# Performance work log

Hardware: AMD Instinct MI355X
Metric: run time of the kernel (lower is better)

## Reference

```python
import jax, jax.numpy as jnp
import numpy as np
from jax import lax

ALPHA_LO = float(np.exp(-1.0 / 5.0))
ALPHA_HI = float(np.exp(-1.0 / 25.0))
THRESHOLD = 1.0


def setup_inputs() -> dict:
    key = jax.random.key(0)
    k1, k2, k3, k4, k5 = jax.random.split(key, 5)
    B, T, I, H = 64, 1024, 512, 512
    x = jax.random.normal(k1, (B, T, I), dtype=jnp.float32)
    # kaiming-uniform-like small init for Linear weight
    bound = 1.0 / np.sqrt(I)
    W = jax.random.uniform(k2, (H, I), minval=-bound, maxval=bound, dtype=jnp.float32)
    alpha = ALPHA_LO + jax.random.uniform(k3, (H,), dtype=jnp.float32) * (ALPHA_HI - ALPHA_LO)
    u0 = jax.random.uniform(k4, (B, H), dtype=jnp.float32)
    s0 = jax.random.uniform(k5, (B, H), dtype=jnp.float32)
    return {"x": x, "W": W, "alpha": alpha, "u0": u0, "s0": s0}


def reference(x, W, alpha, u0, s0):
    # x: [B, T, I], W: [H, I] (torch Linear layout), alpha/u0/s0 over H
    al = jnp.clip(alpha, ALPHA_LO, ALPHA_HI)  # [H]
    Wx = jnp.einsum('bti,hi->bth', x, W)      # [B, T, H]

    def step(carry, wx_t):
        u, s = carry
        u = al * (u - s) + (1.0 - al) * wx_t
        s = (u - THRESHOLD > 0).astype(wx_t.dtype)
        return (u, s), s

    _, spikes = lax.scan(step, (u0, s0), jnp.swapaxes(Wx, 0, 1))  # [T, B, H]
    return jnp.swapaxes(spikes, 0, 1)  # [B, T, H]
```

## Files before the change

### kernel.cpp

```cpp
#include <hip/hip_runtime.h>
#include <hip/hip_bf16.h>


#define ALPHA_LO_F 0.8187307530779818f
#define ALPHA_HI_F 0.9607894391523232f

typedef float v2f __attribute__((ext_vector_type(2)));

#define T_DIM 1024
#define K_DIM 512
#define H_DIM 512
#define CT    256
#define CH    128
#define NCHK  (T_DIM / CT)
#define BK    16
#define APAD  260
#define BPAD  132

__global__ __launch_bounds__(512, 1) void lif_fused(
    const float* __restrict__ x,
    const float* __restrict__ W,
    const float* __restrict__ alpha,
    const float* __restrict__ u0,
    const float* __restrict__ s0,
    float* __restrict__ out)
{
    __shared__ float As[BK][APAD];
    __shared__ float Bs[BK][BPAD];
    __shared__ float u_s[CH], s_s[CH], al_s[CH];

    const int tid = threadIdx.x;
    const int b   = blockIdx.x & 63;
    const int hc  = blockIdx.x >> 6;
    const int h0  = hc * CH;

    if (tid < CH) {
        const int h = h0 + tid;
        float a = alpha[h];
        al_s[tid] = fminf(fmaxf(a, ALPHA_LO_F), ALPHA_HI_F);
        u_s[tid] = u0[(size_t)b * H_DIM + h];
        s_s[tid] = s0[(size_t)b * H_DIM + h];
    }

    const int tm = tid >> 4;
    const int tn = tid & 15;

    const float* xb = x + (size_t)b * T_DIM * K_DIM;
    const float* Wc = W + (size_t)h0 * K_DIM;

    __syncthreads();

    for (int c = 0; c < NCHK; ++c) {
        const int t0 = c * CT;

        v2f acc[8][4] = {};

        for (int k0 = 0; k0 < K_DIM; k0 += BK) {
            #pragma unroll
            for (int r = 0; r < 3; ++r) {
                const int fid = tid + r * 512;
                if (fid < 1024) {
                    const int row = fid >> 2;
                    const int kq  = (fid & 3) * 4;
                    float4 v = *(const float4*)(xb + (size_t)(t0 + row) * K_DIM + k0 + kq);
                    As[kq + 0][row] = v.x;  As[kq + 1][row] = v.y;
                    As[kq + 2][row] = v.z;  As[kq + 3][row] = v.w;
                } else {
                    const int g   = fid - 1024;
                    const int row = g >> 2;
                    const int kq  = (g & 3) * 4;
                    float4 v = *(const float4*)(Wc + (size_t)row * K_DIM + k0 + kq);
                    Bs[kq + 0][row] = v.x;  Bs[kq + 1][row] = v.y;
                    Bs[kq + 2][row] = v.z;  Bs[kq + 3][row] = v.w;
                }
            }
            __syncthreads();

            #pragma unroll
            for (int k = 0; k < BK; ++k) {
                const float* Ak = &As[k][tm * 8];
                const float* Bk = &Bs[k][tn * 8];
                float4 a0 = *(const float4*)(Ak);
                float4 a1 = *(const float4*)(Ak + 4);
                float4 b0 = *(const float4*)(Bk);
                float4 b1 = *(const float4*)(Bk + 4);
                v2f bb[4];
                bb[0] = (v2f){b0.x, b0.y};  bb[1] = (v2f){b0.z, b0.w};
                bb[2] = (v2f){b1.x, b1.y};  bb[3] = (v2f){b1.z, b1.w};
                float a[8] = {a0.x, a0.y, a0.z, a0.w, a1.x, a1.y, a1.z, a1.w};
                #pragma unroll
                for (int i = 0; i < 8; ++i) {
                    v2f ai = (v2f){a[i], a[i]};
                    #pragma unroll
                    for (int jv = 0; jv < 4; ++jv)
                        acc[i][jv] = __builtin_elementwise_fma(ai, bb[jv], acc[i][jv]);
                }
            }
            __syncthreads();
        }

        for (int stage = 0; stage < 32; ++stage) {
            if (tm == stage) {
                const int hb = tn * 8;
                float u[8], s[8], av[8], om[8];
                #pragma unroll
                for (int j = 0; j < 8; ++j) {
                    u[j]  = u_s[hb + j];
                    s[j]  = s_s[hb + j];
                    av[j] = al_s[hb + j];
                    om[j] = 1.0f - av[j];
                }
                #pragma unroll
                for (int i = 0; i < 8; ++i) {
                    float wx[8] = {acc[i][0].x, acc[i][0].y, acc[i][1].x, acc[i][1].y,
                                   acc[i][2].x, acc[i][2].y, acc[i][3].x, acc[i][3].y};
                    #pragma unroll
                    for (int j = 0; j < 8; ++j) {
                        u[j] = av[j] * (u[j] - s[j]) + om[j] * wx[j];
                        s[j] = (u[j] - 1.0f > 0.0f) ? 1.0f : 0.0f;
                    }
                    const int t = t0 + stage * 8 + i;
                    float* orow = out + ((size_t)b * T_DIM + t) * H_DIM + h0 + hb;
                    *(float4*)(orow)     = make_float4(s[0], s[1], s[2], s[3]);
                    *(float4*)(orow + 4) = make_float4(s[4], s[5], s[6], s[7]);
                }
                #pragma unroll
                for (int j = 0; j < 8; ++j) {
                    u_s[hb + j] = u[j];
                    s_s[hb + j] = s[j];
                }
            }
            __syncthreads();
        }
    }
}

extern "C" void kernel_launch(void* const* d_in, const int* in_sizes, int n_in,
                              void* d_out, int out_size, void* d_ws, size_t ws_size,
                              hipStream_t stream) {
    const float* x     = (const float*)d_in[0];
    const float* W     = (const float*)d_in[1];
    const float* alpha = (const float*)d_in[2];
    const float* u0    = (const float*)d_in[3];
    const float* s0    = (const float*)d_in[4];
    float* out = (float*)d_out;

    const int H = in_sizes[2];
    const int B = in_sizes[3] / H;
    const int grid = (H_DIM / CH) * B;

    lif_fused<<<grid, 512, 0, stream>>>(x, W, alpha, u0, s0, out);
}
```

Measured before the change: 726.0 us.

## Double-buffer LDS tiles with register prefetch and halve H chunk per block

Adds register prefetch of the next K tile (and of the next time chunk's first tile) together with double-buffered shared-memory tiles, so global loads overlap the FMA loop and one barrier per K step is dropped. The block is shrunk to 256 threads covering 64 H columns, which doubles the grid and lets two blocks share a CU. In exchange, each x tile is now loaded by twice as many blocks, and the serial recurrence stage still runs one thread row at a time.

```diff
diff --git a/kernel.cpp b/kernel.cpp
--- a/kernel.cpp
+++ b/kernel.cpp
@@ -11,13 +11,13 @@
 #define K_DIM 512
 #define H_DIM 512
 #define CT    256
-#define CH    128
+#define CH    64
 #define NCHK  (T_DIM / CT)
 #define BK    16
 #define APAD  260
-#define BPAD  132
+#define BPAD  68
 
-__global__ __launch_bounds__(512, 1) void lif_fused(
+__global__ __launch_bounds__(256, 2) void lif_fused(
     const float* __restrict__ x,
     const float* __restrict__ W,
     const float* __restrict__ alpha,
@@ -25,8 +25,8 @@
     const float* __restrict__ s0,
     float* __restrict__ out)
 {
-    __shared__ float As[BK][APAD];
-    __shared__ float Bs[BK][BPAD];
+    __shared__ float As[2][BK][APAD];
+    __shared__ float Bs[2][BK][BPAD];
     __shared__ float u_s[CH], s_s[CH], al_s[CH];
 
     const int tid = threadIdx.x;
@@ -42,44 +42,64 @@
         s_s[tid] = s0[(size_t)b * H_DIM + h];
     }
 
-    const int tm = tid >> 4;
-    const int tn = tid & 15;
+    const int tm = tid >> 3;
+    const int tn = tid & 7;
+
+    const int arow = tid >> 2;
+    const int akq  = (tid & 3) * 4;
+    const int brow = tid >> 2;
+    const int bkq  = (tid & 3) * 4;
 
     const float* xb = x + (size_t)b * T_DIM * K_DIM;
     const float* Wc = W + (size_t)h0 * K_DIM;
+
+    float4 aR[4]; float4 bR;
+
+    {
+        #pragma unroll
+        for (int r = 0; r < 4; ++r)
+            aR[r] = *(const float4*)(xb + (size_t)(arow + r * 64) * K_DIM + akq);
+        bR = *(const float4*)(Wc + (size_t)brow * K_DIM + bkq);
+    }
 
     __syncthreads();
 
     for (int c = 0; c < NCHK; ++c) {
         const int t0 = c * CT;
 
+        #pragma unroll
+        for (int r = 0; r < 4; ++r) {
+            const int row = arow + r * 64;
+            As[0][akq + 0][row] = aR[r].x;  As[0][akq + 1][row] = aR[r].y;
+            As[0][akq + 2][row] = aR[r].z;  As[0][akq + 3][row] = aR[r].w;
+        }
+        Bs[0][bkq + 0][brow] = bR.x;  Bs[0][bkq + 1][brow] = bR.y;
+        Bs[0][bkq + 2][brow] = bR.z;  Bs[0][bkq + 3][brow] = bR.w;
+        __syncthreads();
+
         v2f acc[8][4] = {};
 
-        for (int k0 = 0; k0 < K_DIM; k0 += BK) {
-            #pragma unroll
-            for (int r = 0; r < 3; ++r) {
-                const int fid = tid + r * 512;
-                if (fid < 1024) {
-                    const int row = fid >> 2;
-                    const int kq  = (fid & 3) * 4;
-                    float4 v = *(const float4*)(xb + (size_t)(t0 + row) * K_DIM + k0 + kq);
-                    As[kq + 0][row] = v.x;  As[kq + 1][row] = v.y;
-                    As[kq + 2][row] = v.z;  As[kq + 3][row] = v.w;
-                } else {
-                    const int g   = fid - 1024;
-                    const int row = g >> 2;
-                    const int kq  = (g & 3) * 4;
-                    float4 v = *(const float4*)(Wc + (size_t)row * K_DIM + k0 + kq);
-                    Bs[kq + 0][row] = v.x;  Bs[kq + 1][row] = v.y;
-                    Bs[kq + 2][row] = v.z;  Bs[kq + 3][row] = v.w;
-                }
+        for (int kt = 0; kt < K_DIM / BK; ++kt) {
+            const int cur = kt & 1;
+
+            if (kt < K_DIM / BK - 1) {
+                const int k0n = (kt + 1) * BK;
+                #pragma unroll
+                for (int r = 0; r < 4; ++r)
+                    aR[r] = *(const float4*)(xb + (size_t)(t0 + arow + r * 64) * K_DIM + k0n + akq);
+                bR = *(const float4*)(Wc + (size_t)brow * K_DIM + k0n + bkq);
+            } else if (c + 1 < NCHK) {
+                const int t0n = (c + 1) * CT;
+                #pragma unroll
+                for (int r = 0; r < 4; ++r)
+                    aR[r] = *(const float4*)(xb + (size_t)(t0n + arow + r * 64) * K_DIM + akq);
+                bR = *(const float4*)(Wc + (size_t)brow * K_DIM + bkq);
             }
-            __syncthreads();
 
             #pragma unroll
             for (int k = 0; k < BK; ++k) {
-                const float* Ak = &As[k][tm * 8];
-                const float* Bk = &Bs[k][tn * 8];
+                const float* Ak = &As[cur][k][tm * 8];
+                const float* Bk = &Bs[cur][k][tn * 8];
                 float4 a0 = *(const float4*)(Ak);
                 float4 a1 = *(const float4*)(Ak + 4);
                 float4 b0 = *(const float4*)(Bk);
@@ -95,6 +115,18 @@
                     for (int jv = 0; jv < 4; ++jv)
                         acc[i][jv] = __builtin_elementwise_fma(ai, bb[jv], acc[i][jv]);
                 }
+            }
+
+            if (kt < K_DIM / BK - 1) {
+                const int nb = cur ^ 1;
+                #pragma unroll
+                for (int r = 0; r < 4; ++r) {
+                    const int row = arow + r * 64;
+                    As[nb][akq + 0][row] = aR[r].x;  As[nb][akq + 1][row] = aR[r].y;
+                    As[nb][akq + 2][row] = aR[r].z;  As[nb][akq + 3][row] = aR[r].w;
+                }
+                Bs[nb][bkq + 0][brow] = bR.x;  Bs[nb][bkq + 1][brow] = bR.y;
+                Bs[nb][bkq + 2][brow] = bR.z;  Bs[nb][bkq + 3][brow] = bR.w;
             }
             __syncthreads();
         }
@@ -149,5 +181,5 @@
     const int B = in_sizes[3] / H;
     const int grid = (H_DIM / CH) * B;
 
-    lif_fused<<<grid, 512, 0, stream>>>(x, W, alpha, u0, s0, out);
+    lif_fused<<<grid, 256, 0, stream>>>(x, W, alpha, u0, s0, out);
 }
```

After: 2.723 ms. 3.75x slower.
